# Kernel optimization log

Hardware: AMD Instinct MI355X
Metric: run time of the kernel (lower is better)

Reference implementation:

```python
import jax, jax.numpy as jnp
import numpy as np

B, T, D, E, L, MAXP, PRED, TOPK = 128, 2048, 256, 32, 8, 168, 168, 2
INIT_STD = 0.02


def setup_inputs() -> dict:
    key = jax.random.key(0)
    ks = jax.random.split(key, 18)
    n = jax.random.normal
    s = INIT_STD
    inp = {
        "ctx_embed": n(ks[0], (B, T, D), jnp.float32),
        "query_experts": n(ks[1], (E, MAXP, D), jnp.float32) * s,
        "query_pos": n(ks[2], (MAXP, D), jnp.float32) * s,
        "len_emb": n(ks[3], (MAXP + 1, D), jnp.float32),  # nn.Embedding table
        "latents": n(ks[4], (L, D), jnp.float32) * s,
        "w_lat_q": n(ks[5], (D, D), jnp.float32) / np.sqrt(D),
        "w_ctx_k": n(ks[6], (D, D), jnp.float32) / np.sqrt(D),
        "w_ctx_v": n(ks[7], (D, D), jnp.float32) / np.sqrt(D),
        "w_lat_out": n(ks[8], (D, D), jnp.float32) / np.sqrt(D),
        "w_step_q": n(ks[9], (D, D), jnp.float32) / np.sqrt(D),
        "w_lat_k": n(ks[10], (D, D), jnp.float32) / np.sqrt(D),
        "w_lat_v": n(ks[11], (D, D), jnp.float32) / np.sqrt(D),
        "w_step_out": n(ks[12], (D, D), jnp.float32) / np.sqrt(D),
        "gate_w1": n(ks[13], (2 * D, D), jnp.float32) / np.sqrt(2 * D),
        "gate_b1": jnp.zeros((D,), jnp.float32),
        "gate_w2": n(ks[14], (D, E), jnp.float32) / np.sqrt(D),
        "gate_b2": jnp.zeros((E,), jnp.float32),
        "pred_len": PRED,
    }
    return inp


def _sdpa_1head(q, k, v):
    # q: [B,Q,D], k/v: [B,K,D]; single-head scaled dot-product attention
    scale = jnp.asarray(q.shape[-1], q.dtype) ** -0.5
    attn = jax.nn.softmax(jnp.einsum('bqd,bkd->bqk', q, k) * scale, axis=-1)
    return jnp.einsum('bqk,bkd->bqd', attn, v)


def reference(ctx_embed, query_experts, query_pos, len_emb, latents,
              w_lat_q, w_ctx_k, w_ctx_v, w_lat_out,
              w_step_q, w_lat_k, w_lat_v, w_step_out,
              gate_w1, gate_b1, gate_w2, gate_b2, pred_len):
    Bb, Tt, Dd = ctx_embed.shape
    P = pred_len

    # step base: positional queries + pred-length embedding
    pos = query_pos[:P][None]                      # [1,P,D]
    len_vec = len_emb[P][None, None]               # [1,1,D]
    step_base = jnp.broadcast_to(pos + len_vec, (Bb, P, Dd))

    # latent <- context cross-attention
    lat = jnp.broadcast_to(latents[None], (Bb, latents.shape[0], Dd))
    q1 = lat @ w_lat_q
    k1 = ctx_embed @ w_ctx_k
    v1 = ctx_embed @ w_ctx_v
    lat_ctx = _sdpa_1head(q1, k1, v1) @ w_lat_out  # [B,L,D]

    # step <- latent cross-attention
    q2 = step_base @ w_step_q
    k2 = lat_ctx @ w_lat_k
    v2 = lat_ctx @ w_lat_v
    step_ctx = _sdpa_1head(q2, k2, v2) @ w_step_out  # [B,P,D]

    # gating MLP over [step_base, step_ctx]
    gate_inp = jnp.concatenate([step_base, step_ctx], axis=-1)  # [B,P,2D]
    h = jax.nn.gelu(gate_inp @ gate_w1 + gate_b1, approximate=False)
    logits = h @ gate_w2 + gate_b2                               # [B,P,E]

    # top-k masking + softmax (keep top-k logits, others -> -inf)
    topv = jax.lax.top_k(logits, TOPK)[0]
    kth = topv[..., -1:]
    masked = jnp.where(logits >= kth, logits, -jnp.inf)
    weights = jax.nn.softmax(masked, axis=-1)                    # [B,P,E]

    # mixture of expert queries (einsum avoids [B,P,E,D] intermediate)
    queries = jnp.einsum('bpe,epd->bpd', weights, query_experts[:, :P, :])
    return queries
```

## Files before the change

kernel.cpp:

```cpp
#include <hip/hip_runtime.h>
#include <math.h>

#define NB 128
#define NT 2048
#define ND 256
#define NE 32
#define NL 8
#define NP 168
#define SCL 0.0625f

#define OFF_QK   0
#define OFF_LATQ 2048
#define OFF_WVO  4096
#define OFF_WSO1 69632
#define OFF_WVW  135168
#define OFF_G0   200704
#define OFF_Q2S  243712
#define OFF_AV   286720
#define OFF_DEN  2383872
#define OFF_K2   2392064
#define OFF_VW   2654208

typedef __attribute__((ext_vector_type(8))) short short8b;
typedef __attribute__((ext_vector_type(4))) float f32x4;

static __device__ __forceinline__ unsigned short f2bf(float f){
  unsigned u = __float_as_uint(f);
  u += 0x7fffu + ((u >> 16) & 1u);
  return (unsigned short)(u >> 16);
}

static __device__ __forceinline__ short8b pack8(float4 lo, float4 hi){
  short8b r;
  r[0]=(short)f2bf(lo.x); r[1]=(short)f2bf(lo.y); r[2]=(short)f2bf(lo.z); r[3]=(short)f2bf(lo.w);
  r[4]=(short)f2bf(hi.x); r[5]=(short)f2bf(hi.y); r[6]=(short)f2bf(hi.z); r[7]=(short)f2bf(hi.w);
  return r;
}

__global__ __launch_bounds__(256) void pre1(const float* __restrict__ latents,
    const float* __restrict__ wlq, const float* __restrict__ wcv,
    const float* __restrict__ wlo, const float* __restrict__ wso,
    const float* __restrict__ gw1, const float* __restrict__ gb1,
    const float* __restrict__ qpos, const float* __restrict__ lemb,
    const float* __restrict__ wsq, float* __restrict__ ws)
{
  int bid = blockIdx.x, tid = threadIdx.x;
  if (bid < 256){
    const float* a = wcv + bid*ND;
    float acc = 0.f;
    #pragma unroll 8
    for (int k=0;k<ND;k++) acc += a[k]*wlo[k*ND+tid];
    ws[OFF_WVO + bid*ND + tid] = acc;
  } else if (bid < 512){
    int i = bid-256;
    const float* a = wso + i*ND;
    float acc = 0.f;
    #pragma unroll 8
    for (int k=0;k<ND;k++) acc += a[k]*gw1[(ND+k)*ND+tid];
    ws[OFF_WSO1 + i*ND + tid] = acc;
  } else if (bid < 512+NP){
    int p = bid-512;
    float ag = gb1[tid], aq = 0.f;
    #pragma unroll 4
    for (int j=0;j<ND;j++){
      float sb = qpos[p*ND+j] + lemb[NP*ND+j];
      ag += sb*gw1[j*ND+tid];
      aq += sb*wsq[j*ND+tid];
    }
    ws[OFF_G0  + p*ND + tid] = ag;
    ws[OFF_Q2S + p*ND + tid] = aq*SCL;
  } else {
    int l = bid-(512+NP);
    float acc = 0.f;
    #pragma unroll 8
    for (int m=0;m<ND;m++) acc += latents[l*ND+m]*wlq[m*ND+tid];
    ws[OFF_LATQ + l*ND + tid] = acc;
  }
}

__global__ __launch_bounds__(256) void pre2(const float* __restrict__ wck,
                                            const float* __restrict__ wlv,
                                            float* __restrict__ ws)
{
  int bid = blockIdx.x, tid = threadIdx.x;
  if (bid < 256){
    int d = bid;
    float wk = wck[d*ND + tid];
    float part[NL];
    #pragma unroll
    for (int l=0;l<NL;l++) part[l] = ws[OFF_LATQ + l*ND + tid]*wk;
    #pragma unroll
    for (int m=1;m<64;m<<=1){
      #pragma unroll
      for (int l=0;l<NL;l++) part[l] += __shfl_xor(part[l], m);
    }
    __shared__ float red[4][NL];
    if ((tid&63)==0){
      #pragma unroll
      for (int l=0;l<NL;l++) red[tid>>6][l] = part[l];
    }
    __syncthreads();
    if (tid < NL){
      float s = red[0][tid]+red[1][tid]+red[2][tid]+red[3][tid];
      ws[OFF_QK + tid*ND + d] = s*SCL;
    }
  } else {
    int dd = bid - 256;
    const float* a = wlv + dd*ND;
    float acc = 0.f;
    #pragma unroll 8
    for (int k=0;k<ND;k++) acc += a[k]*ws[OFF_WSO1 + k*ND + tid];
    ws[OFF_WVW + dd*ND + tid] = acc;
  }
}

__global__ __launch_bounds__(256) void kA(const float* __restrict__ ctx, float* __restrict__ ws)
{
  __shared__ float ctile[64*256];
  __shared__ float efull[256*8];

  int bid = blockIdx.x;
  int b = bid >> 3, sp = bid & 7;
  int tid = threadIdx.x;
  int wv = tid >> 6, lane = tid & 63;
  int c = lane & 15, g = lane >> 4;
  int dq = lane;

  short8b afrag[8];
  if (c < NL){
    const float* qk = ws + OFF_QK + c*ND + g*8;
    #pragma unroll
    for (int kk=0;kk<8;kk++){
      float4 lo = *(const float4*)(qk + kk*32);
      float4 hi = *(const float4*)(qk + kk*32 + 4);
      afrag[kk] = pack8(lo, hi);
    }
  } else {
    short8b z;
    #pragma unroll
    for (int j=0;j<8;j++) z[j] = 0;
    #pragma unroll
    for (int kk=0;kk<8;kk++) afrag[kk] = z;
  }

  float av[8][4];
  #pragma unroll
  for (int l=0;l<8;l++){
    #pragma unroll
    for (int j=0;j<4;j++) av[l][j] = 0.f;
  }

  const int T0 = sp*256;
  #pragma unroll 1
  for (int sub=0; sub<4; ++sub){
    int rr = wv*16 + c;
    int r7 = rr & 7;
    const float* cp = ctx + ((size_t)(b*NT + T0 + sub*64 + rr))*ND + g*8;
    float4 lo[8], hi[8];
    #pragma unroll
    for (int kk=0;kk<8;kk++){
      lo[kk] = *(const float4*)(cp + kk*32);
      hi[kk] = *(const float4*)(cp + kk*32 + 4);
    }
    float* crow = ctile + rr*256;
    #pragma unroll
    for (int kk=0;kk<8;kk++){
      int slo = 2*g + 8*kk;
      *(float4*)(crow + (((slo  ) ^ r7)<<2)) = lo[kk];
      *(float4*)(crow + (((slo+1) ^ r7)<<2)) = hi[kk];
    }
    f32x4 acc = {0.f,0.f,0.f,0.f};
    #pragma unroll
    for (int kk=0;kk<8;kk++)
      acc = __builtin_amdgcn_mfma_f32_16x16x32_bf16(afrag[kk], pack8(lo[kk],hi[kk]), acc, 0, 0, 0);
    if (g < 2){
      float4 ev = make_float4(__expf(acc[0]),__expf(acc[1]),__expf(acc[2]),__expf(acc[3]));
      *(float4*)&efull[(sub*64 + rr)*8 + g*4] = ev;
    }
    __syncthreads();
    #pragma unroll
    for (int i=0;i<16;i++){
      int tl = wv*16 + i;
      float4 c4 = *(const float4*)(ctile + tl*256 + ((dq ^ (tl&7))<<2));
      const float* ep = efull + (sub*64 + tl)*8;
      float4 e0 = *(const float4*)ep;
      float4 e1 = *(const float4*)(ep+4);
      float e8[8];
      e8[0]=e0.x; e8[1]=e0.y; e8[2]=e0.z; e8[3]=e0.w;
      e8[4]=e1.x; e8[5]=e1.y; e8[6]=e1.z; e8[7]=e1.w;
      #pragma unroll
      for (int l=0;l<8;l++){
        av[l][0] += e8[l]*c4.x;
        av[l][1] += e8[l]*c4.y;
        av[l][2] += e8[l]*c4.z;
        av[l][3] += e8[l]*c4.w;
      }
    }
    __syncthreads();
  }

  float* red = ctile;
  #pragma unroll
  for (int l=0;l<8;l++)
    *(float4*)(red + (((l*4 + wv)*64 + dq)<<2)) = make_float4(av[l][0],av[l][1],av[l][2],av[l][3]);

  if (wv == 0){
    float dpart[8];
    #pragma unroll
    for (int l=0;l<8;l++) dpart[l] = 0.f;
    #pragma unroll
    for (int q=0;q<4;q++){
      const float* ep = efull + (q*64 + lane)*8;
      float4 e0 = *(const float4*)ep;
      float4 e1 = *(const float4*)(ep+4);
      dpart[0]+=e0.x; dpart[1]+=e0.y; dpart[2]+=e0.z; dpart[3]+=e0.w;
      dpart[4]+=e1.x; dpart[5]+=e1.y; dpart[6]+=e1.z; dpart[7]+=e1.w;
    }
    #pragma unroll
    for (int m=1;m<64;m<<=1){
      #pragma unroll
      for (int l=0;l<8;l++) dpart[l] += __shfl_xor(dpart[l], m);
    }
    if (lane == 0){
      #pragma unroll
      for (int l=0;l<8;l++) ws[OFF_DEN + bid*8 + l] = dpart[l];
    }
  }
  __syncthreads();

  #pragma unroll
  for (int rep=0; rep<2; ++rep){
    int lidx = tid + rep*256;
    int l = lidx >> 6, d2 = lidx & 63;
    float4 s0 = *(const float4*)(red + (((l*4 + 0)*64 + d2)<<2));
    float4 s1 = *(const float4*)(red + (((l*4 + 1)*64 + d2)<<2));
    float4 s2 = *(const float4*)(red + (((l*4 + 2)*64 + d2)<<2));
    float4 s3 = *(const float4*)(red + (((l*4 + 3)*64 + d2)<<2));
    float4 o;
    o.x = s0.x+s1.x+s2.x+s3.x;
    o.y = s0.y+s1.y+s2.y+s3.y;
    o.z = s0.z+s1.z+s2.z+s3.z;
    o.w = s0.w+s1.w+s2.w+s3.w;
    *(float4*)&ws[OFF_AV + ((size_t)(bid*8 + l))*ND + d2*4] = o;
  }
}

__global__ __launch_bounds__(256) void kB1(const float* __restrict__ wlk,
                                           float* __restrict__ ws)
{
  int bid = blockIdx.x;
  int b = bid >> 1, half = bid & 1;
  int d = threadIdx.x;
  __shared__ float avnT[256][8];
  __shared__ float latT[256][8];

  float dent[8];
  #pragma unroll
  for (int l=0;l<8;l++){
    float s = 0.f;
    #pragma unroll
    for (int sp=0;sp<8;sp++) s += ws[OFF_DEN + (b*8+sp)*8 + l];
    dent[l] = s;
  }
  float av8[8];
  #pragma unroll
  for (int l=0;l<8;l++){
    float s = 0.f;
    #pragma unroll
    for (int sp=0;sp<8;sp++) s += ws[OFF_AV + ((size_t)((b*8+sp)*8 + l))*ND + d];
    av8[l] = s / dent[l];
  }
  *(float4*)&avnT[d][0] = make_float4(av8[0],av8[1],av8[2],av8[3]);
  *(float4*)&avnT[d][4] = make_float4(av8[4],av8[5],av8[6],av8[7]);
  __syncthreads();

  float lc[8];
  #pragma unroll
  for (int l=0;l<8;l++) lc[l] = 0.f;
  #pragma unroll 8
  for (int dd=0;dd<ND;dd++){
    float w = ws[OFF_WVO + dd*ND + d];
    float4 a0 = *(const float4*)&avnT[dd][0];
    float4 a1 = *(const float4*)&avnT[dd][4];
    lc[0]+=a0.x*w; lc[1]+=a0.y*w; lc[2]+=a0.z*w; lc[3]+=a0.w*w;
    lc[4]+=a1.x*w; lc[5]+=a1.y*w; lc[6]+=a1.z*w; lc[7]+=a1.w*w;
  }
  *(float4*)&latT[d][0] = make_float4(lc[0],lc[1],lc[2],lc[3]);
  *(float4*)&latT[d][4] = make_float4(lc[4],lc[5],lc[6],lc[7]);
  __syncthreads();

  const float* w3 = half ? (ws + OFF_WVW) : wlk;
  float o8[8];
  #pragma unroll
  for (int l=0;l<8;l++) o8[l] = 0.f;
  #pragma unroll 8
  for (int dd=0;dd<ND;dd++){
    float w = w3[dd*ND + d];
    float4 a0 = *(const float4*)&latT[dd][0];
    float4 a1 = *(const float4*)&latT[dd][4];
    o8[0]+=a0.x*w; o8[1]+=a0.y*w; o8[2]+=a0.z*w; o8[3]+=a0.w*w;
    o8[4]+=a1.x*w; o8[5]+=a1.y*w; o8[6]+=a1.z*w; o8[7]+=a1.w*w;
  }
  size_t obase = (half ? OFF_VW : OFF_K2) + (size_t)b*8*ND + d;
  #pragma unroll
  for (int l=0;l<8;l++) ws[obase + l*ND] = o8[l];
}

__global__ __launch_bounds__(256) void kB2(const float* __restrict__ ws,
    const float* __restrict__ gw2, const float* __restrict__ gb2,
    const float* __restrict__ qe, float* __restrict__ out)
{
  int bid = blockIdx.x;
  int b = bid / 6, p0 = (bid % 6)*28;
  int tid = threadIdx.x;

  __shared__ float q2h[28][260];
  __shared__ float k2s[8][260];
  __shared__ float vws[8][260];
  __shared__ float wexp[28][8];
  __shared__ float lg[28][33];
  __shared__ float4 sel[28];

  #pragma unroll
  for (int i=0;i<7;i++){
    int idx = tid + i*256;
    int r = idx >> 6, c4 = idx & 63;
    *(float4*)&q2h[r][c4*4] = *(const float4*)&ws[OFF_Q2S + (p0+r)*ND + c4*4];
  }
  #pragma unroll
  for (int i=0;i<2;i++){
    int idx = tid + i*256;
    int l = idx >> 6, c4 = idx & 63;
    *(float4*)&k2s[l][c4*4] = *(const float4*)&ws[OFF_K2 + (b*8+l)*ND + c4*4];
    *(float4*)&vws[l][c4*4] = *(const float4*)&ws[OFF_VW + (b*8+l)*ND + c4*4];
  }
  __syncthreads();

  {
    int pp = tid >> 3, l1 = tid & 7;
    if (pp < 28){
      float s2 = 0.f;
      #pragma unroll 8
      for (int i=0;i<64;i++){
        float4 qa = *(const float4*)&q2h[pp][4*i];
        float4 kb = *(const float4*)&k2s[l1][4*i];
        s2 += qa.x*kb.x + qa.y*kb.y + qa.z*kb.z + qa.w*kb.w;
      }
      float e2 = __expf(s2);
      float den = e2;
      den += __shfl_xor(den,1); den += __shfl_xor(den,2); den += __shfl_xor(den,4);
      wexp[pp][l1] = e2/den;
    }
  }
  __syncthreads();

  {
    float vcol[8];
    #pragma unroll
    for (int l=0;l<8;l++) vcol[l] = vws[l][tid];
    #pragma unroll 4
    for (int p=0;p<28;p++){
      float4 w0 = *(const float4*)&wexp[p][0];
      float4 w1v = *(const float4*)&wexp[p][4];
      float x = ws[OFF_G0 + (p0+p)*ND + tid]
              + w0.x*vcol[0]+w0.y*vcol[1]+w0.z*vcol[2]+w0.w*vcol[3]
              + w1v.x*vcol[4]+w1v.y*vcol[5]+w1v.z*vcol[6]+w1v.w*vcol[7];
      q2h[p][tid] = 0.5f*x*(1.f+erff(x*0.70710678118654752f));
    }
  }
  __syncthreads();

  {
    int e = tid & 31, pq = tid >> 5;
    if (pq < 7){
      float b2v = gb2[e];
      float a0=b2v, a1=b2v, a2=b2v, a3=b2v;
      for (int cc=0;cc<ND;cc+=4){
        float w20 = gw2[(cc+0)*NE + e];
        float w21 = gw2[(cc+1)*NE + e];
        float w22 = gw2[(cc+2)*NE + e];
        float w23 = gw2[(cc+3)*NE + e];
        float4 h0 = *(const float4*)&q2h[pq*4+0][cc];
        float4 h1 = *(const float4*)&q2h[pq*4+1][cc];
        float4 h2 = *(const float4*)&q2h[pq*4+2][cc];
        float4 h3 = *(const float4*)&q2h[pq*4+3][cc];
        a0 += h0.x*w20 + h0.y*w21 + h0.z*w22 + h0.w*w23;
        a1 += h1.x*w20 + h1.y*w21 + h1.z*w22 + h1.w*w23;
        a2 += h2.x*w20 + h2.y*w21 + h2.z*w22 + h2.w*w23;
        a3 += h3.x*w20 + h3.y*w21 + h3.z*w22 + h3.w*w23;
      }
      lg[pq*4+0][e] = a0;
      lg[pq*4+1][e] = a1;
      lg[pq*4+2][e] = a2;
      lg[pq*4+3][e] = a3;
    }
  }
  __syncthreads();

  if (tid < 28){
    float m1 = -1e30f, m2 = -1e30f;
    int e1 = 0, ee2 = 0;
    for (int e3=0;e3<NE;e3++){
      float v = lg[tid][e3];
      if (v > m1){ m2 = m1; ee2 = e1; m1 = v; e1 = e3; }
      else if (v > m2){ m2 = v; ee2 = e3; }
    }
    float z = __expf(m2 - m1);
    float inv = 1.f/(1.f+z);
    sel[tid] = make_float4(__int_as_float(e1), __int_as_float(ee2), inv, z*inv);
  }
  __syncthreads();

  for (int p=0;p<28;p++){
    float4 s = sel[p];
    int e1 = __float_as_int(s.x), ee2 = __float_as_int(s.y);
    float q1v = qe[((size_t)e1*NP + (p0+p))*ND + tid];
    float q2v = qe[((size_t)ee2*NP + (p0+p))*ND + tid];
    out[((size_t)b*NP + (p0+p))*ND + tid] = s.z*q1v + s.w*q2v;
  }
}

extern "C" void kernel_launch(void* const* d_in, const int* in_sizes, int n_in,
                              void* d_out, int out_size, void* d_ws, size_t ws_size,
                              hipStream_t stream)
{
  const float* ctx  = (const float*)d_in[0];
  const float* qe   = (const float*)d_in[1];
  const float* qpos = (const float*)d_in[2];
  const float* lemb = (const float*)d_in[3];
  const float* lat  = (const float*)d_in[4];
  const float* wlq  = (const float*)d_in[5];
  const float* wck  = (const float*)d_in[6];
  const float* wcv  = (const float*)d_in[7];
  const float* wlo  = (const float*)d_in[8];
  const float* wsq  = (const float*)d_in[9];
  const float* wlk  = (const float*)d_in[10];
  const float* wlv  = (const float*)d_in[11];
  const float* wso  = (const float*)d_in[12];
  const float* gw1  = (const float*)d_in[13];
  const float* gb1  = (const float*)d_in[14];
  const float* gw2  = (const float*)d_in[15];
  const float* gb2  = (const float*)d_in[16];
  float* out = (float*)d_out;
  float* ws  = (float*)d_ws;

  pre1<<<512+NP+NL, 256, 0, stream>>>(lat, wlq, wcv, wlo, wso, gw1, gb1, qpos, lemb, wsq, ws);
  pre2<<<512, 256, 0, stream>>>(wck, wlv, ws);
  kA  <<<NB*8, 256, 0, stream>>>(ctx, ws);
  kB1 <<<NB*2, 256, 0, stream>>>(wlk, ws);
  kB2 <<<NB*6, 256, 0, stream>>>(ws, gw2, gb2, qe, out);
}
```

Before: 154.0 us.

## Merge prep kernels, reassociate weight products into per-batch chains, use packed bf16 conversion

Drops the second prep kernel. The latent-query-times-key-weight product is now computed by reassociating the matmul order, so the prep work fits in one launch. Instead of precomputing the fused w_lat_v·w_step_out·gate_w1 weight product, kB1 applies the three matrices in sequence for each batch on the value half. kA's accumulation is recast into float2 vectors so the compiler can emit packed FMAs, and the bf16 conversion now uses the library intrinsic. This removes one launch and its serial dependency, but it adds per-batch matvec work and a longer serial chain in the value-half blocks of kB1.

Measured after the change: 163.2 us. 6.0% more time.

```diff
diff --git a/kernel.cpp b/kernel.cpp
--- a/kernel.cpp
+++ b/kernel.cpp
@@ -1,4 +1,5 @@
 #include <hip/hip_runtime.h>
+#include <hip/hip_bf16.h>
 #include <math.h>
 
 #define NB 128
@@ -10,10 +11,7 @@
 #define SCL 0.0625f
 
 #define OFF_QK   0
-#define OFF_LATQ 2048
 #define OFF_WVO  4096
-#define OFF_WSO1 69632
-#define OFF_WVW  135168
 #define OFF_G0   200704
 #define OFF_Q2S  243712
 #define OFF_AV   286720
@@ -23,23 +21,23 @@
 
 typedef __attribute__((ext_vector_type(8))) short short8b;
 typedef __attribute__((ext_vector_type(4))) float f32x4;
-
-static __device__ __forceinline__ unsigned short f2bf(float f){
-  unsigned u = __float_as_uint(f);
-  u += 0x7fffu + ((u >> 16) & 1u);
-  return (unsigned short)(u >> 16);
+typedef __attribute__((ext_vector_type(2))) float f32x2;
+
+static __device__ __forceinline__ short bfc(float f){
+  __hip_bfloat16 h = __float2bfloat16(f);
+  return *reinterpret_cast<short*>(&h);
 }
 
 static __device__ __forceinline__ short8b pack8(float4 lo, float4 hi){
   short8b r;
-  r[0]=(short)f2bf(lo.x); r[1]=(short)f2bf(lo.y); r[2]=(short)f2bf(lo.z); r[3]=(short)f2bf(lo.w);
-  r[4]=(short)f2bf(hi.x); r[5]=(short)f2bf(hi.y); r[6]=(short)f2bf(hi.z); r[7]=(short)f2bf(hi.w);
+  r[0]=bfc(lo.x); r[1]=bfc(lo.y); r[2]=bfc(lo.z); r[3]=bfc(lo.w);
+  r[4]=bfc(hi.x); r[5]=bfc(hi.y); r[6]=bfc(hi.z); r[7]=bfc(hi.w);
   return r;
 }
 
-__global__ __launch_bounds__(256) void pre1(const float* __restrict__ latents,
-    const float* __restrict__ wlq, const float* __restrict__ wcv,
-    const float* __restrict__ wlo, const float* __restrict__ wso,
+__global__ __launch_bounds__(256) void preA(const float* __restrict__ latents,
+    const float* __restrict__ wlq, const float* __restrict__ wck,
+    const float* __restrict__ wcv, const float* __restrict__ wlo,
     const float* __restrict__ gw1, const float* __restrict__ gb1,
     const float* __restrict__ qpos, const float* __restrict__ lemb,
     const float* __restrict__ wsq, float* __restrict__ ws)
@@ -51,15 +49,8 @@
     #pragma unroll 8
     for (int k=0;k<ND;k++) acc += a[k]*wlo[k*ND+tid];
     ws[OFF_WVO + bid*ND + tid] = acc;
-  } else if (bid < 512){
-    int i = bid-256;
-    const float* a = wso + i*ND;
-    float acc = 0.f;
-    #pragma unroll 8
-    for (int k=0;k<ND;k++) acc += a[k]*gw1[(ND+k)*ND+tid];
-    ws[OFF_WSO1 + i*ND + tid] = acc;
-  } else if (bid < 512+NP){
-    int p = bid-512;
+  } else if (bid < 256+NP){
+    int p = bid-256;
     float ag = gb1[tid], aq = 0.f;
     #pragma unroll 4
     for (int j=0;j<ND;j++){
@@ -70,31 +61,27 @@
     ws[OFF_G0  + p*ND + tid] = ag;
     ws[OFF_Q2S + p*ND + tid] = aq*SCL;
   } else {
-    int l = bid-(512+NP);
-    float acc = 0.f;
+    int d = bid-(256+NP);
+    __shared__ float ck[ND];
+    __shared__ float red[4][NL];
+    ck[tid] = wck[d*ND + tid];
+    __syncthreads();
+    const float* wrow = wlq + tid*ND;
+    float macc = 0.f;
     #pragma unroll 8
-    for (int m=0;m<ND;m++) acc += latents[l*ND+m]*wlq[m*ND+tid];
-    ws[OFF_LATQ + l*ND + tid] = acc;
-  }
-}
-
-__global__ __launch_bounds__(256) void pre2(const float* __restrict__ wck,
-                                            const float* __restrict__ wlv,
-                                            float* __restrict__ ws)
-{
-  int bid = blockIdx.x, tid = threadIdx.x;
-  if (bid < 256){
-    int d = bid;
-    float wk = wck[d*ND + tid];
+    for (int k4=0;k4<64;k4++){
+      float4 w4 = *(const float4*)(wrow + k4*4);
+      float4 c4 = *(const float4*)(ck + k4*4);
+      macc += w4.x*c4.x + w4.y*c4.y + w4.z*c4.z + w4.w*c4.w;
+    }
     float part[NL];
     #pragma unroll
-    for (int l=0;l<NL;l++) part[l] = ws[OFF_LATQ + l*ND + tid]*wk;
+    for (int l=0;l<NL;l++) part[l] = latents[l*ND + tid]*macc;
     #pragma unroll
     for (int m=1;m<64;m<<=1){
       #pragma unroll
       for (int l=0;l<NL;l++) part[l] += __shfl_xor(part[l], m);
     }
-    __shared__ float red[4][NL];
     if ((tid&63)==0){
       #pragma unroll
       for (int l=0;l<NL;l++) red[tid>>6][l] = part[l];
@@ -104,13 +91,6 @@
       float s = red[0][tid]+red[1][tid]+red[2][tid]+red[3][tid];
       ws[OFF_QK + tid*ND + d] = s*SCL;
     }
-  } else {
-    int dd = bid - 256;
-    const float* a = wlv + dd*ND;
-    float acc = 0.f;
-    #pragma unroll 8
-    for (int k=0;k<ND;k++) acc += a[k]*ws[OFF_WSO1 + k*ND + tid];
-    ws[OFF_WVW + dd*ND + tid] = acc;
   }
 }
 
@@ -143,12 +123,9 @@
     for (int kk=0;kk<8;kk++) afrag[kk] = z;
   }
 
-  float av[8][4];
-  #pragma unroll
-  for (int l=0;l<8;l++){
-    #pragma unroll
-    for (int j=0;j<4;j++) av[l][j] = 0.f;
-  }
+  f32x2 av[8][2];
+  #pragma unroll
+  for (int l=0;l<8;l++){ av[l][0] = (f32x2){0.f,0.f}; av[l][1] = (f32x2){0.f,0.f}; }
 
   const int T0 = sp*256;
   #pragma unroll 1
@@ -182,19 +159,18 @@
     for (int i=0;i<16;i++){
       int tl = wv*16 + i;
       float4 c4 = *(const float4*)(ctile + tl*256 + ((dq ^ (tl&7))<<2));
+      f32x2 cA = {c4.x, c4.y}, cB = {c4.z, c4.w};
       const float* ep = efull + (sub*64 + tl)*8;
       float4 e0 = *(const float4*)ep;
       float4 e1 = *(const float4*)(ep+4);
-      float e8[8];
-      e8[0]=e0.x; e8[1]=e0.y; e8[2]=e0.z; e8[3]=e0.w;
-      e8[4]=e1.x; e8[5]=e1.y; e8[6]=e1.z; e8[7]=e1.w;
-      #pragma unroll
-      for (int l=0;l<8;l++){
-        av[l][0] += e8[l]*c4.x;
-        av[l][1] += e8[l]*c4.y;
-        av[l][2] += e8[l]*c4.z;
-        av[l][3] += e8[l]*c4.w;
-      }
+      av[0][0] += e0.x*cA; av[0][1] += e0.x*cB;
+      av[1][0] += e0.y*cA; av[1][1] += e0.y*cB;
+      av[2][0] += e0.z*cA; av[2][1] += e0.z*cB;
+      av[3][0] += e0.w*cA; av[3][1] += e0.w*cB;
+      av[4][0] += e1.x*cA; av[4][1] += e1.x*cB;
+      av[5][0] += e1.y*cA; av[5][1] += e1.y*cB;
+      av[6][0] += e1.z*cA; av[6][1] += e1.z*cB;
+      av[7][0] += e1.w*cA; av[7][1] += e1.w*cB;
     }
     __syncthreads();
   }
@@ -202,7 +178,7 @@
   float* red = ctile;
   #pragma unroll
   for (int l=0;l<8;l++)
-    *(float4*)(red + (((l*4 + wv)*64 + dq)<<2)) = make_float4(av[l][0],av[l][1],av[l][2],av[l][3]);
+    *(float4*)(red + (((l*4 + wv)*64 + dq)<<2)) = make_float4(av[l][0][0],av[l][0][1],av[l][1][0],av[l][1][1]);
 
   if (wv == 0){
     float dpart[8];
@@ -246,13 +222,16 @@
 }
 
 __global__ __launch_bounds__(256) void kB1(const float* __restrict__ wlk,
+                                           const float* __restrict__ wlv,
+                                           const float* __restrict__ wso,
+                                           const float* __restrict__ gw1,
                                            float* __restrict__ ws)
 {
   int bid = blockIdx.x;
   int b = bid >> 1, half = bid & 1;
   int d = threadIdx.x;
-  __shared__ float avnT[256][8];
-  __shared__ float latT[256][8];
+  __shared__ float bufA[256][8];
+  __shared__ float bufB[256][8];
 
   float dent[8];
   #pragma unroll
@@ -270,40 +249,80 @@
     for (int sp=0;sp<8;sp++) s += ws[OFF_AV + ((size_t)((b*8+sp)*8 + l))*ND + d];
     av8[l] = s / dent[l];
   }
-  *(float4*)&avnT[d][0] = make_float4(av8[0],av8[1],av8[2],av8[3]);
-  *(float4*)&avnT[d][4] = make_float4(av8[4],av8[5],av8[6],av8[7]);
-  __syncthreads();
-
-  float lc[8];
-  #pragma unroll
-  for (int l=0;l<8;l++) lc[l] = 0.f;
-  #pragma unroll 8
-  for (int dd=0;dd<ND;dd++){
-    float w = ws[OFF_WVO + dd*ND + d];
-    float4 a0 = *(const float4*)&avnT[dd][0];
-    float4 a1 = *(const float4*)&avnT[dd][4];
-    lc[0]+=a0.x*w; lc[1]+=a0.y*w; lc[2]+=a0.z*w; lc[3]+=a0.w*w;
-    lc[4]+=a1.x*w; lc[5]+=a1.y*w; lc[6]+=a1.z*w; lc[7]+=a1.w*w;
-  }
-  *(float4*)&latT[d][0] = make_float4(lc[0],lc[1],lc[2],lc[3]);
-  *(float4*)&latT[d][4] = make_float4(lc[4],lc[5],lc[6],lc[7]);
-  __syncthreads();
-
-  const float* w3 = half ? (ws + OFF_WVW) : wlk;
-  float o8[8];
-  #pragma unroll
-  for (int l=0;l<8;l++) o8[l] = 0.f;
-  #pragma unroll 8
-  for (int dd=0;dd<ND;dd++){
-    float w = w3[dd*ND + d];
-    float4 a0 = *(const float4*)&latT[dd][0];
-    float4 a1 = *(const float4*)&latT[dd][4];
-    o8[0]+=a0.x*w; o8[1]+=a0.y*w; o8[2]+=a0.z*w; o8[3]+=a0.w*w;
-    o8[4]+=a1.x*w; o8[5]+=a1.y*w; o8[6]+=a1.z*w; o8[7]+=a1.w*w;
-  }
-  size_t obase = (half ? OFF_VW : OFF_K2) + (size_t)b*8*ND + d;
-  #pragma unroll
-  for (int l=0;l<8;l++) ws[obase + l*ND] = o8[l];
+  *(float4*)&bufA[d][0] = make_float4(av8[0],av8[1],av8[2],av8[3]);
+  *(float4*)&bufA[d][4] = make_float4(av8[4],av8[5],av8[6],av8[7]);
+  __syncthreads();
+
+  {
+    float lc[8];
+    #pragma unroll
+    for (int l=0;l<8;l++) lc[l] = 0.f;
+    #pragma unroll 8
+    for (int dd=0;dd<ND;dd++){
+      float w = ws[OFF_WVO + dd*ND + d];
+      float4 a0 = *(const float4*)&bufA[dd][0];
+      float4 a1 = *(const float4*)&bufA[dd][4];
+      lc[0]+=a0.x*w; lc[1]+=a0.y*w; lc[2]+=a0.z*w; lc[3]+=a0.w*w;
+      lc[4]+=a1.x*w; lc[5]+=a1.y*w; lc[6]+=a1.z*w; lc[7]+=a1.w*w;
+    }
+    __syncthreads();
+    *(float4*)&bufB[d][0] = make_float4(lc[0],lc[1],lc[2],lc[3]);
+    *(float4*)&bufB[d][4] = make_float4(lc[4],lc[5],lc[6],lc[7]);
+  }
+  __syncthreads();
+
+#define CHAIN(DST, SRC, WPTR)                                                   \
+  do {                                                                           \
+    float o8_[8];                                                                \
+    _Pragma("unroll")                                                            \
+    for (int l=0;l<8;l++) o8_[l] = 0.f;                                          \
+    _Pragma("unroll 8")                                                          \
+    for (int dd=0;dd<ND;dd++){                                                   \
+      float w = (WPTR)[dd*ND + d];                                               \
+      float4 a0 = *(const float4*)&SRC[dd][0];                                   \
+      float4 a1 = *(const float4*)&SRC[dd][4];                                   \
+      o8_[0]+=a0.x*w; o8_[1]+=a0.y*w; o8_[2]+=a0.z*w; o8_[3]+=a0.w*w;            \
+      o8_[4]+=a1.x*w; o8_[5]+=a1.y*w; o8_[6]+=a1.z*w; o8_[7]+=a1.w*w;            \
+    }                                                                            \
+    __syncthreads();                                                             \
+    *(float4*)&DST[d][0] = make_float4(o8_[0],o8_[1],o8_[2],o8_[3]);             \
+    *(float4*)&DST[d][4] = make_float4(o8_[4],o8_[5],o8_[6],o8_[7]);             \
+    __syncthreads();                                                             \
+  } while(0)
+
+  if (half == 0){
+    float o8[8];
+    #pragma unroll
+    for (int l=0;l<8;l++) o8[l] = 0.f;
+    #pragma unroll 8
+    for (int dd=0;dd<ND;dd++){
+      float w = wlk[dd*ND + d];
+      float4 a0 = *(const float4*)&bufB[dd][0];
+      float4 a1 = *(const float4*)&bufB[dd][4];
+      o8[0]+=a0.x*w; o8[1]+=a0.y*w; o8[2]+=a0.z*w; o8[3]+=a0.w*w;
+      o8[4]+=a1.x*w; o8[5]+=a1.y*w; o8[6]+=a1.z*w; o8[7]+=a1.w*w;
+    }
+    #pragma unroll
+    for (int l=0;l<8;l++) ws[OFF_K2 + (size_t)b*8*ND + l*ND + d] = o8[l];
+  } else {
+    CHAIN(bufA, bufB, wlv);
+    CHAIN(bufB, bufA, wso);
+    const float* gw1b = gw1 + (size_t)ND*ND;
+    float o8[8];
+    #pragma unroll
+    for (int l=0;l<8;l++) o8[l] = 0.f;
+    #pragma unroll 8
+    for (int dd=0;dd<ND;dd++){
+      float w = gw1b[dd*ND + d];
+      float4 a0 = *(const float4*)&bufB[dd][0];
+      float4 a1 = *(const float4*)&bufB[dd][4];
+      o8[0]+=a0.x*w; o8[1]+=a0.y*w; o8[2]+=a0.z*w; o8[3]+=a0.w*w;
+      o8[4]+=a1.x*w; o8[5]+=a1.y*w; o8[6]+=a1.z*w; o8[7]+=a1.w*w;
+    }
+    #pragma unroll
+    for (int l=0;l<8;l++) ws[OFF_VW + (size_t)b*8*ND + l*ND + d] = o8[l];
+  }
+#undef CHAIN
 }
 
 __global__ __launch_bounds__(256) void kB2(const float* __restrict__ ws,
@@ -444,9 +463,8 @@
   float* out = (float*)d_out;
   float* ws  = (float*)d_ws;
 
-  pre1<<<512+NP+NL, 256, 0, stream>>>(lat, wlq, wcv, wlo, wso, gw1, gb1, qpos, lemb, wsq, ws);
-  pre2<<<512, 256, 0, stream>>>(wck, wlv, ws);
+  preA<<<256+NP+256, 256, 0, stream>>>(lat, wlq, wck, wcv, wlo, gw1, gb1, qpos, lemb, wsq, ws);
   kA  <<<NB*8, 256, 0, stream>>>(ctx, ws);
-  kB1 <<<NB*2, 256, 0, stream>>>(wlk, ws);
+  kB1 <<<NB*2, 256, 0, stream>>>(wlk, wlv, wso, gw1, ws);
   kB2 <<<NB*6, 256, 0, stream>>>(ws, gw2, gb2, qe, out);
 }
```

## Double-buffer context tiles via direct global-to-LDS loads in kA

Applied to the files above, without the earlier changes.

Replaces the register-staged context load and LDS store with global_load_lds direct-to-LDS transfers into a double buffer. The next 64-row tile is prefetched while the current one is processed. Block-wide __syncthreads inside the loop are replaced by per-wave waitcnt, relying on each wave touching only its own rows. This aims to overlap HBM loads with the MFMA score and exp-weighted accumulation work, at the cost of doubling LDS per block (lower occupancy) and depending on fragile manual wait counts.

After: 282.4 us. 1.83x slower.

```diff
diff --git a/kernel.cpp b/kernel.cpp
--- a/kernel.cpp
+++ b/kernel.cpp
@@ -116,7 +116,7 @@
 
 __global__ __launch_bounds__(256) void kA(const float* __restrict__ ctx, float* __restrict__ ws)
 {
-  __shared__ float ctile[64*256];
+  __shared__ float buf[2][64*256];
   __shared__ float efull[256*8];
 
   int bid = blockIdx.x;
@@ -125,6 +125,7 @@
   int wv = tid >> 6, lane = tid & 63;
   int c = lane & 15, g = lane >> 4;
   int dq = lane;
+  const int T0 = sp*256;
 
   short8b afrag[8];
   if (c < NL){
@@ -150,38 +151,54 @@
     for (int j=0;j<4;j++) av[l][j] = 0.f;
   }
 
-  const int T0 = sp*256;
-  #pragma unroll 1
+  int rr = wv*16 + c, r7 = rr & 7;
+
+#define STAGE(SUBN, BUFI) do{                                                     \
+    _Pragma("unroll")                                                             \
+    for (int i_=0;i_<16;i_++){                                                    \
+      int r_ = wv*16 + i_;                                                        \
+      const float* gsrc_ = ctx + ((size_t)(b*NT + T0 + (SUBN)*64 + r_))*ND        \
+                               + ((lane ^ (r_&7))<<2);                            \
+      __builtin_amdgcn_global_load_lds(                                           \
+          (const __attribute__((address_space(1))) void*)gsrc_,                   \
+          (__attribute__((address_space(3))) void*)&buf[BUFI][r_*256], 16, 0, 0); \
+    }                                                                             \
+  }while(0)
+
+  STAGE(0, 0);
+
+  #pragma unroll
   for (int sub=0; sub<4; ++sub){
-    int rr = wv*16 + c;
-    int r7 = rr & 7;
-    const float* cp = ctx + ((size_t)(b*NT + T0 + sub*64 + rr))*ND + g*8;
-    float4 lo[8], hi[8];
+    int cur = sub & 1;
+    asm volatile("s_waitcnt lgkmcnt(0)" ::: "memory");
+    __builtin_amdgcn_sched_barrier(0);
+    if (sub < 3){
+      STAGE(sub+1, cur^1);
+      asm volatile("s_waitcnt vmcnt(16)" ::: "memory");
+    } else {
+      asm volatile("s_waitcnt vmcnt(0)" ::: "memory");
+    }
+    __builtin_amdgcn_sched_barrier(0);
+
+    const float* bb = &buf[cur][0];
+    f32x4 acc = {0.f,0.f,0.f,0.f};
     #pragma unroll
     for (int kk=0;kk<8;kk++){
-      lo[kk] = *(const float4*)(cp + kk*32);
-      hi[kk] = *(const float4*)(cp + kk*32 + 4);
-    }
-    float* crow = ctile + rr*256;
-    #pragma unroll
-    for (int kk=0;kk<8;kk++){
-      int slo = 2*g + 8*kk;
-      *(float4*)(crow + (((slo  ) ^ r7)<<2)) = lo[kk];
-      *(float4*)(crow + (((slo+1) ^ r7)<<2)) = hi[kk];
-    }
-    f32x4 acc = {0.f,0.f,0.f,0.f};
-    #pragma unroll
-    for (int kk=0;kk<8;kk++)
-      acc = __builtin_amdgcn_mfma_f32_16x16x32_bf16(afrag[kk], pack8(lo[kk],hi[kk]), acc, 0, 0, 0);
+      int sA = 2*g + 8*kk;
+      float4 lo = *(const float4*)(bb + rr*256 + (((sA  ) ^ r7)<<2));
+      float4 hi = *(const float4*)(bb + rr*256 + (((sA+1) ^ r7)<<2));
+      acc = __builtin_amdgcn_mfma_f32_16x16x32_bf16(afrag[kk], pack8(lo,hi), acc, 0, 0, 0);
+    }
     if (g < 2){
       float4 ev = make_float4(__expf(acc[0]),__expf(acc[1]),__expf(acc[2]),__expf(acc[3]));
       *(float4*)&efull[(sub*64 + rr)*8 + g*4] = ev;
     }
-    __syncthreads();
+    asm volatile("s_waitcnt lgkmcnt(0)" ::: "memory");
+    __builtin_amdgcn_sched_barrier(0);
     #pragma unroll
     for (int i=0;i<16;i++){
       int tl = wv*16 + i;
-      float4 c4 = *(const float4*)(ctile + tl*256 + ((dq ^ (tl&7))<<2));
+      float4 c4 = *(const float4*)(bb + tl*256 + ((dq ^ (tl&7))<<2));
       const float* ep = efull + (sub*64 + tl)*8;
       float4 e0 = *(const float4*)ep;
       float4 e1 = *(const float4*)(ep+4);
@@ -196,10 +213,12 @@
         av[l][3] += e8[l]*c4.w;
       }
     }
-    __syncthreads();
-  }
-
-  float* red = ctile;
+  }
+#undef STAGE
+
+  __syncthreads();
+
+  float* red = &buf[0][0];
   #pragma unroll
   for (int l=0;l<8;l++)
     *(float4*)(red + (((l*4 + wv)*64 + dq)<<2)) = make_float4(av[l][0],av[l][1],av[l][2],av[l][3]);
```

## Split context attention across more blocks with per-wave row tiles and no block barriers

Applied to the files above, without the earlier changes.

The context cross-attention kernel now uses 16 blocks per batch instead of 8, each covering 128 tokens with half the shared memory. Each wave loads its own 8 rows with coalesced full-row reads, builds the MFMA operands from shared memory, and accumulates without block-wide barriers inside the loop. The partial-sum workspace grows, so the downstream reducer sums 16 partials per batch, which adds some reduction traffic.

Result: slower. 165.6 us (+7.5%).

```diff
diff --git a/kernel.cpp b/kernel.cpp
--- a/kernel.cpp
+++ b/kernel.cpp
@@ -17,9 +17,9 @@
 #define OFF_G0   200704
 #define OFF_Q2S  243712
 #define OFF_AV   286720
-#define OFF_DEN  2383872
-#define OFF_K2   2392064
-#define OFF_VW   2654208
+#define OFF_DEN  4481024
+#define OFF_K2   4497408
+#define OFF_VW   4759552
 
 typedef __attribute__((ext_vector_type(8))) short short8b;
 typedef __attribute__((ext_vector_type(4))) float f32x4;
@@ -116,15 +116,16 @@
 
 __global__ __launch_bounds__(256) void kA(const float* __restrict__ ctx, float* __restrict__ ws)
 {
-  __shared__ float ctile[64*256];
-  __shared__ float efull[256*8];
+  __shared__ float ctile[32*256];
+  __shared__ float efull[128*8];
 
   int bid = blockIdx.x;
-  int b = bid >> 3, sp = bid & 7;
+  int b = bid >> 4, sp = bid & 15;
   int tid = threadIdx.x;
   int wv = tid >> 6, lane = tid & 63;
   int c = lane & 15, g = lane >> 4;
   int dq = lane;
+  int c7 = c & 7;
 
   short8b afrag[8];
   if (c < NL){
@@ -150,54 +151,52 @@
     for (int j=0;j<4;j++) av[l][j] = 0.f;
   }
 
-  const int T0 = sp*256;
-  #pragma unroll 1
+  const float* rbase = ctx + ((size_t)(b*NT + sp*128 + wv*8))*ND;
+  float* myrows = ctile + wv*8*256;
+
+  #pragma unroll 2
   for (int sub=0; sub<4; ++sub){
-    int rr = wv*16 + c;
-    int r7 = rr & 7;
-    const float* cp = ctx + ((size_t)(b*NT + T0 + sub*64 + rr))*ND + g*8;
-    float4 lo[8], hi[8];
+    const float* rs = rbase + (size_t)sub*32*ND;
+    float4 st[8];
+    #pragma unroll
+    for (int i=0;i<8;i++)
+      st[i] = *(const float4*)(rs + (size_t)i*ND + lane*4);
+    #pragma unroll
+    for (int i=0;i<8;i++)
+      *(float4*)(myrows + i*256 + ((lane ^ i)<<2)) = st[i];
+
+    f32x4 acc = {0.f,0.f,0.f,0.f};
+    const float* brow = myrows + c7*256;
     #pragma unroll
     for (int kk=0;kk<8;kk++){
-      lo[kk] = *(const float4*)(cp + kk*32);
-      hi[kk] = *(const float4*)(cp + kk*32 + 4);
-    }
-    float* crow = ctile + rr*256;
-    #pragma unroll
-    for (int kk=0;kk<8;kk++){
-      int slo = 2*g + 8*kk;
-      *(float4*)(crow + (((slo  ) ^ r7)<<2)) = lo[kk];
-      *(float4*)(crow + (((slo+1) ^ r7)<<2)) = hi[kk];
-    }
-    f32x4 acc = {0.f,0.f,0.f,0.f};
-    #pragma unroll
-    for (int kk=0;kk<8;kk++)
-      acc = __builtin_amdgcn_mfma_f32_16x16x32_bf16(afrag[kk], pack8(lo[kk],hi[kk]), acc, 0, 0, 0);
-    if (g < 2){
+      int sA = 2*g + 8*kk;
+      float4 lo = *(const float4*)(brow + (((sA  ) ^ c7)<<2));
+      float4 hi = *(const float4*)(brow + (((sA+1) ^ c7)<<2));
+      acc = __builtin_amdgcn_mfma_f32_16x16x32_bf16(afrag[kk], pack8(lo,hi), acc, 0, 0, 0);
+    }
+    if (g < 2 && c < 8){
       float4 ev = make_float4(__expf(acc[0]),__expf(acc[1]),__expf(acc[2]),__expf(acc[3]));
-      *(float4*)&efull[(sub*64 + rr)*8 + g*4] = ev;
-    }
-    __syncthreads();
-    #pragma unroll
-    for (int i=0;i<16;i++){
-      int tl = wv*16 + i;
-      float4 c4 = *(const float4*)(ctile + tl*256 + ((dq ^ (tl&7))<<2));
-      const float* ep = efull + (sub*64 + tl)*8;
+      *(float4*)&efull[(sub*32 + wv*8 + c)*8 + g*4] = ev;
+    }
+
+    #pragma unroll
+    for (int i=0;i<8;i++){
+      float4 c4 = *(const float4*)(myrows + i*256 + ((dq ^ i)<<2));
+      const float* ep = efull + (sub*32 + wv*8 + i)*8;
       float4 e0 = *(const float4*)ep;
       float4 e1 = *(const float4*)(ep+4);
-      float e8[8];
-      e8[0]=e0.x; e8[1]=e0.y; e8[2]=e0.z; e8[3]=e0.w;
-      e8[4]=e1.x; e8[5]=e1.y; e8[6]=e1.z; e8[7]=e1.w;
-      #pragma unroll
-      for (int l=0;l<8;l++){
-        av[l][0] += e8[l]*c4.x;
-        av[l][1] += e8[l]*c4.y;
-        av[l][2] += e8[l]*c4.z;
-        av[l][3] += e8[l]*c4.w;
-      }
-    }
-    __syncthreads();
-  }
+      av[0][0]+=e0.x*c4.x; av[0][1]+=e0.x*c4.y; av[0][2]+=e0.x*c4.z; av[0][3]+=e0.x*c4.w;
+      av[1][0]+=e0.y*c4.x; av[1][1]+=e0.y*c4.y; av[1][2]+=e0.y*c4.z; av[1][3]+=e0.y*c4.w;
+      av[2][0]+=e0.z*c4.x; av[2][1]+=e0.z*c4.y; av[2][2]+=e0.z*c4.z; av[2][3]+=e0.z*c4.w;
+      av[3][0]+=e0.w*c4.x; av[3][1]+=e0.w*c4.y; av[3][2]+=e0.w*c4.z; av[3][3]+=e0.w*c4.w;
+      av[4][0]+=e1.x*c4.x; av[4][1]+=e1.x*c4.y; av[4][2]+=e1.x*c4.z; av[4][3]+=e1.x*c4.w;
+      av[5][0]+=e1.y*c4.x; av[5][1]+=e1.y*c4.y; av[5][2]+=e1.y*c4.z; av[5][3]+=e1.y*c4.w;
+      av[6][0]+=e1.z*c4.x; av[6][1]+=e1.z*c4.y; av[6][2]+=e1.z*c4.z; av[6][3]+=e1.z*c4.w;
+      av[7][0]+=e1.w*c4.x; av[7][1]+=e1.w*c4.y; av[7][2]+=e1.w*c4.z; av[7][3]+=e1.w*c4.w;
+    }
+  }
+
+  __syncthreads();
 
   float* red = ctile;
   #pragma unroll
@@ -209,7 +208,7 @@
     #pragma unroll
     for (int l=0;l<8;l++) dpart[l] = 0.f;
     #pragma unroll
-    for (int q=0;q<4;q++){
+    for (int q=0;q<2;q++){
       const float* ep = efull + (q*64 + lane)*8;
       float4 e0 = *(const float4*)ep;
       float4 e1 = *(const float4*)(ep+4);
@@ -256,20 +255,26 @@
 
   float dent[8];
   #pragma unroll
-  for (int l=0;l<8;l++){
-    float s = 0.f;
-    #pragma unroll
-    for (int sp=0;sp<8;sp++) s += ws[OFF_DEN + (b*8+sp)*8 + l];
-    dent[l] = s;
+  for (int l=0;l<8;l++) dent[l] = 0.f;
+  #pragma unroll 4
+  for (int sp=0;sp<16;sp++){
+    const float* dp = ws + OFF_DEN + (size_t)(b*16+sp)*8;
+    float4 d0 = *(const float4*)dp;
+    float4 d1 = *(const float4*)(dp+4);
+    dent[0]+=d0.x; dent[1]+=d0.y; dent[2]+=d0.z; dent[3]+=d0.w;
+    dent[4]+=d1.x; dent[5]+=d1.y; dent[6]+=d1.z; dent[7]+=d1.w;
   }
   float av8[8];
   #pragma unroll
-  for (int l=0;l<8;l++){
-    float s = 0.f;
-    #pragma unroll
-    for (int sp=0;sp<8;sp++) s += ws[OFF_AV + ((size_t)((b*8+sp)*8 + l))*ND + d];
-    av8[l] = s / dent[l];
-  }
+  for (int l=0;l<8;l++) av8[l] = 0.f;
+  #pragma unroll 2
+  for (int sp=0;sp<16;sp++){
+    size_t base = OFF_AV + ((size_t)(b*16+sp))*8*ND + d;
+    #pragma unroll
+    for (int l=0;l<8;l++) av8[l] += ws[base + (size_t)l*ND];
+  }
+  #pragma unroll
+  for (int l=0;l<8;l++) av8[l] /= dent[l];
   *(float4*)&avnT[d][0] = make_float4(av8[0],av8[1],av8[2],av8[3]);
   *(float4*)&avnT[d][4] = make_float4(av8[4],av8[5],av8[6],av8[7]);
   __syncthreads();
@@ -331,8 +336,8 @@
   for (int i=0;i<2;i++){
     int idx = tid + i*256;
     int l = idx >> 6, c4 = idx & 63;
-    *(float4*)&k2s[l][c4*4] = *(const float4*)&ws[OFF_K2 + (b*8+l)*ND + c4*4];
-    *(float4*)&vws[l][c4*4] = *(const float4*)&ws[OFF_VW + (b*8+l)*ND + c4*4];
+    *(float4*)&k2s[l][c4*4] = *(const float4*)&ws[OFF_K2 + (size_t)(b*8+l)*ND + c4*4];
+    *(float4*)&vws[l][c4*4] = *(const float4*)&ws[OFF_VW + (size_t)(b*8+l)*ND + c4*4];
   }
   __syncthreads();
 
@@ -446,7 +451,7 @@
 
   pre1<<<512+NP+NL, 256, 0, stream>>>(lat, wlq, wcv, wlo, wso, gw1, gb1, qpos, lemb, wsq, ws);
   pre2<<<512, 256, 0, stream>>>(wck, wlv, ws);
-  kA  <<<NB*8, 256, 0, stream>>>(ctx, ws);
+  kA  <<<2048, 256, 0, stream>>>(ctx, ws);
   kB1 <<<NB*2, 256, 0, stream>>>(wlk, ws);
   kB2 <<<NB*6, 256, 0, stream>>>(ws, gw2, gb2, qe, out);
 }
```
